# Kernel tuning notes

Hardware: AMD Instinct MI355X
Metric: run time of the kernel (lower is better)

The kernel has to match this reference:

```python
import jax, jax.numpy as jnp
import numpy as np

B, N, D = 2, 2048, 1024
H, HD = 16, 64
SCALE = HD ** (-0.5)


def setup_inputs() -> dict:
    key = jax.random.key(0)
    k1, k2, k3, k4 = jax.random.split(key, 4)
    x = jax.random.normal(k1, (B, N, D), dtype=jnp.float32)
    mask = jax.random.randint(k2, (B, 1, N, N), 0, 2) == 1  # bool, True = masked out
    W_qkv = jax.random.normal(k3, (D, 3 * H * HD), dtype=jnp.float32) * (D ** -0.5)
    W_out = jax.random.normal(k4, (H * HD, D), dtype=jnp.float32) * ((H * HD) ** -0.5)
    b_out = jnp.zeros((D,), dtype=jnp.float32)
    return {"x": x, "mask": mask, "W_qkv": W_qkv, "W_out": W_out, "b_out": b_out}


def reference(x, mask, W_qkv, W_out, b_out):
    b, n, _ = x.shape
    qkv = x @ W_qkv                                  # [b, n, 3*h*hd]
    q, k, v = jnp.split(qkv, 3, axis=-1)
    split_heads = lambda t: t.reshape(b, n, H, HD).transpose(0, 2, 1, 3)  # b h n d
    q, k, v = split_heads(q), split_heads(k), split_heads(v)
    scores = jnp.einsum('bhid,bhjd->bhij', q, k) * SCALE
    scores = jnp.where(mask, jnp.finfo(scores.dtype).min, scores)
    attn = jax.nn.softmax(scores, axis=-1)           # dropout p=0 -> identity
    out = jnp.einsum('bhij,bhjd->bhid', attn, v)     # [b, h, n, hd]
    out = out.transpose(0, 2, 1, 3).reshape(b, n, H * HD)
    return out @ W_out + b_out
```

## Files before the change

kernel.cpp:

```cpp
#include <hip/hip_runtime.h>
#include <stdint.h>

typedef unsigned short u16;
typedef short short8 __attribute__((ext_vector_type(8)));
typedef float f32x4 __attribute__((ext_vector_type(4)));
typedef float f32x16 __attribute__((ext_vector_type(16)));
typedef unsigned int uint2v __attribute__((ext_vector_type(2)));

#define K2E 0.18033688011112042f

__device__ __forceinline__ u16 f2bf(float f) {
  union { float f; uint32_t u; } v;
  v.f = f;
  uint32_t u = v.u;
  u += 0x7FFFu + ((u >> 16) & 1u);
  return (u16)(u >> 16);
}

__device__ __forceinline__ uint32_t cvtpk(float lo, float hi) {
  uint32_t r;
  asm("v_cvt_pk_bf16_f32 %0, %1, %2" : "=v"(r) : "v"(lo), "v"(hi));
  return r;
}

__device__ __forceinline__ float exp2a(float x) {
  float r;
  asm("v_exp_f32 %0, %1" : "=v"(r) : "v"(x));
  return r;
}

__device__ __forceinline__ float mask_keep(float p, uint32_t zm, int oc) {
  int m = (int)(zm << (31 - oc)) >> 31;
  return __uint_as_float(__float_as_uint(p) & (uint32_t)m);
}

__device__ __forceinline__ float row_add2(float x) {
  uint2v r = __builtin_amdgcn_permlane32_swap(__float_as_uint(x), __float_as_uint(x), false, false);
  return __uint_as_float(r.x) + __uint_as_float(r.y);
}

__device__ __forceinline__ void gld_lds16(const u16* src, char* dst) {
  __builtin_amdgcn_global_load_lds((const __attribute__((address_space(1))) void*)src,
                                   (__attribute__((address_space(3))) void*)dst, 16, 0, 0);
}

__device__ __forceinline__ void pack_frags(const f32x16& v, short8& fa, short8& fb) {
  union U { uint32_t w[4]; short8 v8; };
  uint32_t X0 = cvtpk(v[0], v[1]),   X1 = cvtpk(v[2], v[3]);
  uint32_t Y0 = cvtpk(v[4], v[5]),   Y1 = cvtpk(v[6], v[7]);
  uint32_t X2 = cvtpk(v[8], v[9]),   X3 = cvtpk(v[10], v[11]);
  uint32_t Y2 = cvtpk(v[12], v[13]), Y3 = cvtpk(v[14], v[15]);
  uint2v r0 = __builtin_amdgcn_permlane32_swap(X0, Y0, false, false);
  uint2v r1 = __builtin_amdgcn_permlane32_swap(X1, Y1, false, false);
  uint2v r2 = __builtin_amdgcn_permlane32_swap(X2, Y2, false, false);
  uint2v r3 = __builtin_amdgcn_permlane32_swap(X3, Y3, false, false);
  U ua; ua.w[0] = r0.x; ua.w[1] = r1.x; ua.w[2] = r0.y; ua.w[3] = r1.y; fa = ua.v8;
  U ub; ub.w[0] = r2.x; ub.w[1] = r3.x; ub.w[2] = r2.y; ub.w[3] = r3.y; fb = ub.v8;
}


__global__ __launch_bounds__(256) void k_cvt_x(const float* __restrict__ x,
                                               u16* __restrict__ xb, int n4) {
  int g = blockIdx.x * 256 + threadIdx.x;
  if (g >= n4) return;
  float4 v = ((const float4*)x)[g];
  ushort4 o;
  o.x = f2bf(v.x); o.y = f2bf(v.y); o.z = f2bf(v.z); o.w = f2bf(v.w);
  ((ushort4*)xb)[g] = o;
}

__global__ __launch_bounds__(256) void k_transpose_bf(const float* __restrict__ src,
                                                      u16* __restrict__ dst, int R, int C) {
  __shared__ float t[32][33];
  int c0 = blockIdx.x * 32, r0 = blockIdx.y * 32;
  int tx = threadIdx.x, ty = threadIdx.y;
#pragma unroll
  for (int i = 0; i < 4; ++i)
    t[ty + 8 * i][tx] = src[(size_t)(r0 + ty + 8 * i) * C + c0 + tx];
  __syncthreads();
#pragma unroll
  for (int i = 0; i < 4; ++i)
    dst[(size_t)(c0 + ty + 8 * i) * R + r0 + tx] = f2bf(t[tx][ty + 8 * i]);
}

__global__ __launch_bounds__(256) void k_mask_pack(const int* __restrict__ m,
                                                   uint32_t* __restrict__ w, int n) {
  int g = blockIdx.x * 256 + threadIdx.x;
  if (g >= n) return;
  unsigned long long bal = __ballot(m[g] != 0);
  int lane = threadIdx.x & 63;
  if (lane == 0) w[g >> 5] = (uint32_t)bal;
  else if (lane == 32) w[g >> 5] = (uint32_t)(bal >> 32);
}


#define GSTAGE(BUF, H, KT2)                                              \
  {                                                                      \
    char* dA_ = lds + (BUF) * 32768 + (H) * 16384 + (w << 11);           \
    const u16* a_ = As + (((KT2) << 6) + ((H) << 5));                    \
    const u16* b_ = Bs + (((KT2) << 6) + ((H) << 5));                    \
    gld_lds16(a_, dA_);                                                  \
    gld_lds16(a_ + (K << 4), dA_ + 1024);                                \
    gld_lds16(b_, dA_ + 8192);                                           \
    gld_lds16(b_ + (K << 4), dA_ + 9216);                                \
  }

#define PHASE(KT, H, VMS, DOSTAGE)                                                        \
  {                                                                                       \
    asm volatile("s_waitcnt vmcnt(" VMS ")" ::: "memory");                                \
    __builtin_amdgcn_sched_barrier(0);                                                    \
    __builtin_amdgcn_s_barrier();                                                         \
    __builtin_amdgcn_sched_barrier(0);                                                    \
    const char* rb_ = lds + ((KT) & 1) * 32768 + (H) * 16384;                             \
    short8 af[4], bfr[4];                                                                 \
    _Pragma("unroll")                                                                     \
    for (int mi = 0; mi < 4; ++mi) {                                                      \
      int row = wm * 64 + mi * 16 + lr;                                                   \
      af[mi] = *(const short8*)(rb_ + row * 64 + ((lg ^ ((row >> 1) & 3)) << 4));         \
    }                                                                                     \
    _Pragma("unroll")                                                                     \
    for (int ni = 0; ni < 4; ++ni) {                                                      \
      int row = wn * 64 + ni * 16 + lr;                                                   \
      bfr[ni] = *(const short8*)(rb_ + 8192 + row * 64 + ((lg ^ ((row >> 1) & 3)) << 4)); \
    }                                                                                     \
    asm volatile("s_waitcnt lgkmcnt(0)" ::: "memory");                                    \
    __builtin_amdgcn_sched_barrier(0);                                                    \
    __builtin_amdgcn_s_barrier();                                                         \
    __builtin_amdgcn_sched_barrier(0);                                                    \
    if (DOSTAGE) GSTAGE((KT) & 1, H, (KT) + 2);                                           \
    __builtin_amdgcn_s_setprio(1);                                                        \
    _Pragma("unroll")                                                                     \
    for (int mi = 0; mi < 4; ++mi)                                                        \
      _Pragma("unroll")                                                                   \
      for (int ni = 0; ni < 4; ++ni)                                                      \
        acc[mi][ni] =                                                                     \
            __builtin_amdgcn_mfma_f32_16x16x32_bf16(af[mi], bfr[ni], acc[mi][ni], 0, 0, 0); \
    __builtin_amdgcn_s_setprio(0);                                                        \
  }

__device__ __forceinline__ void gemm_core(const u16* __restrict__ A,
                                          const u16* __restrict__ Bt,
                                          int K, int m0, int n0,
                                          f32x4 (&acc)[4][4], char* lds) {
  const int t = threadIdx.x;
  const int l = t & 63;
  const int w = t >> 6;
  const int wm = w >> 1, wn = w & 1;
  const int lr = l & 15, lg = l >> 4;
  const int r0 = (w << 5) + (l >> 2);
  const int c = (l & 3) ^ ((r0 >> 1) & 3);
  const u16* As = A + (size_t)(m0 + r0) * K + c * 8;
  const u16* Bs = Bt + (size_t)(n0 + r0) * K + c * 8;
  const int nkt = K >> 6;

  GSTAGE(0, 0, 0);
  GSTAGE(0, 1, 0);
  GSTAGE(1, 0, 1);
  GSTAGE(1, 1, 1);

#pragma unroll 1
  for (int kt = 0; kt < nkt - 2; ++kt) {
    PHASE(kt, 0, "12", true);
    PHASE(kt, 1, "12", true);
  }
  PHASE(nkt - 2, 0, "12", false);
  PHASE(nkt - 2, 1, "8", false);
  PHASE(nkt - 1, 0, "4", false);
  PHASE(nkt - 1, 1, "0", false);
}

__global__ __launch_bounds__(256, 2) void k_gemm_qkv(const u16* __restrict__ xb,
                                                     const u16* __restrict__ wqT,
                                                     u16* __restrict__ Qb,
                                                     u16* __restrict__ Kb,
                                                     u16* __restrict__ VT) {
  __shared__ char lds[65536] __attribute__((aligned(128)));
  int n0 = blockIdx.x * 128, m0 = blockIdx.y * 128;
  f32x4 acc[4][4] = {};
  gemm_core(xb, wqT, 1024, m0, n0, acc, lds);
  const int l = threadIdx.x & 63, w = threadIdx.x >> 6;
  const int wm = w >> 1, wn = w & 1;
  const int lr = l & 15, lg = l >> 4;
#pragma unroll
  for (int mi = 0; mi < 4; ++mi)
#pragma unroll
    for (int ni = 0; ni < 4; ++ni)
#pragma unroll
      for (int r = 0; r < 4; ++r) {
        int m = m0 + wm * 64 + mi * 16 + lg * 4 + r;
        int n = n0 + wn * 64 + ni * 16 + lr;
        int b = m >> 11, seq = m & 2047;
        u16 v = f2bf(acc[mi][ni][r]);
        if (n < 1024) {
          Qb[((size_t)((b << 4) + (n >> 6)) * 2048 + seq) * 64 + (n & 63)] = v;
        } else if (n < 2048) {
          int nn = n - 1024;
          Kb[((size_t)((b << 4) + (nn >> 6)) * 2048 + seq) * 64 + (nn & 63)] = v;
        } else {
          int nn = n - 2048;
          VT[((size_t)((b << 4) + (nn >> 6)) * 64 + (nn & 63)) * 2048 + seq] = v;
        }
      }
}

__global__ __launch_bounds__(256, 2) void k_gemm_out(const u16* __restrict__ ao,
                                                     const u16* __restrict__ woT,
                                                     const float* __restrict__ bias,
                                                     float* __restrict__ out) {
  __shared__ char lds[65536] __attribute__((aligned(128)));
  int n0 = blockIdx.x * 128, m0 = blockIdx.y * 128;
  f32x4 acc[4][4] = {};
  gemm_core(ao, woT, 1024, m0, n0, acc, lds);
  const int l = threadIdx.x & 63, w = threadIdx.x >> 6;
  const int wm = w >> 1, wn = w & 1;
  const int lr = l & 15, lg = l >> 4;
#pragma unroll
  for (int mi = 0; mi < 4; ++mi)
#pragma unroll
    for (int ni = 0; ni < 4; ++ni)
#pragma unroll
      for (int r = 0; r < 4; ++r) {
        int m = m0 + wm * 64 + mi * 16 + lg * 4 + r;
        int n = n0 + wn * 64 + ni * 16 + lr;
        out[(size_t)m * 1024 + n] = acc[mi][ni][r] + bias[n];
      }
}

__global__ __launch_bounds__(512, 4) void k_attn(const u16* __restrict__ Qg,
                                                 const u16* __restrict__ Kg,
                                                 const u16* __restrict__ Vg,
                                                 const uint32_t* __restrict__ maskw,
                                                 u16* __restrict__ AO) {
  __shared__ char lds[65536] __attribute__((aligned(128)));
  const int bid = blockIdx.x;
  const int qt = bid & 15;
  const int hd = (bid >> 4) & 15;
  const int b = bid >> 8;
  const int bh = (b << 4) + hd;
  const int tx = threadIdx.x, l = tx & 63, w = tx >> 6;
  const int wq = w & 3, kvh = w >> 2;
  const int l31 = l & 31, h = l >> 5;
  const int hx4 = (h ^ (l & 7)) << 4;
  const int sc8 = ((l & 7) ^ (l >> 3)) << 3;
  const int lr8 = l >> 3;

  const u16* Qp = Qg + (size_t)bh * 131072;
  const int q = qt * 128 + wq * 32 + l31;
  const int kv0 = kvh << 10;

  const u16* kg = Kg + (size_t)bh * 131072 + (size_t)(kv0 + 16 * wq + lr8) * 64 + sc8;
  const u16* vg = Vg + (size_t)bh * 131072 + (size_t)(16 * wq + lr8) * 2048 + kv0 + sc8;
  const uint2v* mp = (const uint2v*)(maskw + ((size_t)(b << 11) + q) * 64) + (kvh << 4);

  short8 qf[4];
#pragma unroll
  for (int s = 0; s < 4; ++s)
    qf[s] = *(const short8*)(Qp + (size_t)q * 64 + s * 16 + h * 8);

  f32x16 Oa[2] = {};
  float l_run = 0.f;
  char* ldsH = lds + (kvh << 15);

#define STAGE(BSEL, TT)                                       \
  {                                                           \
    char* base_ = ldsH + (BSEL) * 16384 + (wq << 11);         \
    const u16* k_ = kg + ((size_t)(TT) << 12);                \
    const u16* v_ = vg + ((size_t)(TT) << 6);                 \
    gld_lds16(k_, base_);                                     \
    gld_lds16(k_ + 512, base_ + 1024);                        \
    gld_lds16(v_, base_ + 8192);                              \
    gld_lds16(v_ + 16384, base_ + 9216);                      \
  }

  STAGE(0, 0);

#pragma unroll 1
  for (int tt = 0; tt < 16; ++tt) {
    __syncthreads();
    if (tt + 1 < 16) STAGE((tt + 1) & 1, tt + 1);
    const uint2v mm = mp[tt];
    const char* kbase = ldsH + (tt & 1) * 16384 + l31 * 128;
    const char* vbase = kbase + 8192;

    f32x16 sa = {}, sb = {};
    __builtin_amdgcn_s_setprio(1);
#pragma unroll
    for (int s = 0; s < 4; ++s) {
      short8 k0 = *(const short8*)(kbase + ((s << 5) ^ hx4));
      short8 k1 = *(const short8*)(kbase + 4096 + ((s << 5) ^ hx4));
      sa = __builtin_amdgcn_mfma_f32_32x32x16_bf16(k0, qf[s], sa, 0, 0, 0);
      sb = __builtin_amdgcn_mfma_f32_32x32x16_bf16(k1, qf[s], sb, 0, 0, 0);
    }
    __builtin_amdgcn_s_setprio(0);

    const uint32_t zm0 = ~(mm.x >> (4 * h));
    const uint32_t zm1 = ~(mm.y >> (4 * h));
    float s0 = 0.f, s1 = 0.f, s2 = 0.f, s3 = 0.f;
#pragma unroll
    for (int r = 0; r < 16; r += 2) {
      const int oc = (r & 3) + 8 * (r >> 2);
      float e0 = mask_keep(exp2a(sa[r] * K2E), zm0, oc);
      float e1 = mask_keep(exp2a(sb[r] * K2E), zm1, oc);
      float e2 = mask_keep(exp2a(sa[r + 1] * K2E), zm0, oc + 1);
      float e3 = mask_keep(exp2a(sb[r + 1] * K2E), zm1, oc + 1);
      sa[r] = e0; sb[r] = e1; sa[r + 1] = e2; sb[r + 1] = e3;
      s0 += e0; s1 += e1; s2 += e2; s3 += e3;
    }
    l_run += row_add2((s0 + s2) + (s1 + s3));

    short8 pf[4];
    pack_frags(sa, pf[0], pf[1]);
    pack_frags(sb, pf[2], pf[3]);

    __builtin_amdgcn_s_setprio(1);
#pragma unroll
    for (int cc = 0; cc < 4; ++cc) {
      short8 v0 = *(const short8*)(vbase + ((cc << 5) ^ hx4));
      short8 v1 = *(const short8*)(vbase + 4096 + ((cc << 5) ^ hx4));
      Oa[0] = __builtin_amdgcn_mfma_f32_32x32x16_bf16(v0, pf[cc], Oa[0], 0, 0, 0);
      Oa[1] = __builtin_amdgcn_mfma_f32_32x32x16_bf16(v1, pf[cc], Oa[1], 0, 0, 0);
    }
    __builtin_amdgcn_s_setprio(0);
  }
#undef STAGE

  __syncthreads();
  float* cb = (float*)lds;
  if (kvh) {
#pragma unroll
    for (int r = 0; r < 32; ++r)
      cb[((wq << 5) + r) * 64 + l] = Oa[r >> 4][r & 15];
    cb[8192 + (wq << 6) + l] = l_run;
  }
  __syncthreads();
  if (!kvh) {
#pragma unroll
    for (int r = 0; r < 32; ++r)
      Oa[r >> 4][r & 15] += cb[((wq << 5) + r) * 64 + l];
    float lt = l_run + cb[8192 + (wq << 6) + l];
    float inv = 1.0f / fmaxf(lt, 1e-30f);
    u16* orow = AO + ((size_t)(b << 11) + q) * 1024 + hd * 64 + h * 4;
#pragma unroll
    for (int dt = 0; dt < 2; ++dt)
#pragma unroll
      for (int rq = 0; rq < 4; ++rq) {
        uint32_t w0 = cvtpk(Oa[dt][4 * rq + 0] * inv, Oa[dt][4 * rq + 1] * inv);
        uint32_t w1 = cvtpk(Oa[dt][4 * rq + 2] * inv, Oa[dt][4 * rq + 3] * inv);
        *(uint32_t*)(orow + dt * 32 + rq * 8) = w0;
        *(uint32_t*)(orow + dt * 32 + rq * 8 + 2) = w1;
      }
  }
}


extern "C" void kernel_launch(void* const* d_in, const int* in_sizes, int n_in,
                              void* d_out, int out_size, void* d_ws, size_t ws_size,
                              hipStream_t stream) {
  const float* x = (const float*)d_in[0];
  const int* mask = (const int*)d_in[1];
  const float* Wqkv = (const float*)d_in[2];
  const float* Wout = (const float*)d_in[3];
  const float* bout = (const float*)d_in[4];
  float* out = (float*)d_out;
  char* ws = (char*)d_ws;
  const size_t MB = 1u << 20;
  if (ws_size < 49 * MB) return;

  u16* xb = (u16*)(ws);
  u16* wqT = (u16*)(ws + 8 * MB);
  u16* woT = (u16*)(ws + 14 * MB);
  uint32_t* mw = (uint32_t*)(ws + 16 * MB);
  u16* Qb = (u16*)(ws + 17 * MB);
  u16* Kb = (u16*)(ws + 25 * MB);
  u16* VT = (u16*)(ws + 33 * MB);
  u16* AO = (u16*)(ws + 41 * MB);

  k_cvt_x<<<4096, 256, 0, stream>>>(x, xb, 1048576);
  k_transpose_bf<<<dim3(96, 32), dim3(32, 8), 0, stream>>>(Wqkv, wqT, 1024, 3072);
  k_transpose_bf<<<dim3(32, 32), dim3(32, 8), 0, stream>>>(Wout, woT, 1024, 1024);
  k_mask_pack<<<32768, 256, 0, stream>>>(mask, mw, 8388608);
  k_gemm_qkv<<<dim3(24, 32), 256, 0, stream>>>(xb, wqT, Qb, Kb, VT);
  k_attn<<<512, 512, 0, stream>>>(Qb, Kb, VT, mw, AO);
  k_gemm_out<<<dim3(8, 32), 256, 0, stream>>>(AO, woT, bout, out);
}
```

Measured before the change: 150.6 us.

## Triple-buffer GEMM pipeline, fold softmax scale into Q, compute row sums via MFMA

The GEMM core switches from a 2x2 half-tile double buffer to a three-stage ring of 16KB stages (48KB LDS) with occupancy raised to 3 blocks per CU. In attention, the exp2 scale factor is folded into Q at the QKV epilogue, masking uses a bfe+bfi pair, and softmax row sums are accumulated with an extra MFMA against a ones vector instead of VALU adds and a permlane swap. Together these target LDS-limited occupancy and VALU work in the softmax. In exchange the attention loop issues more MFMA work, Q rounding now includes the scale, and the GEMM loop hard-codes K=1024.

```diff
diff --git a/kernel.cpp b/kernel.cpp
--- a/kernel.cpp
+++ b/kernel.cpp
@@ -29,14 +29,11 @@
   return r;
 }
 
-__device__ __forceinline__ float mask_keep(float p, uint32_t zm, int oc) {
-  int m = (int)(zm << (31 - oc)) >> 31;
-  return __uint_as_float(__float_as_uint(p) & (uint32_t)m);
-}
-
-__device__ __forceinline__ float row_add2(float x) {
-  uint2v r = __builtin_amdgcn_permlane32_swap(__float_as_uint(x), __float_as_uint(x), false, false);
-  return __uint_as_float(r.x) + __uint_as_float(r.y);
+__device__ __forceinline__ float mask_zero(float p, uint32_t zm, int oc) {
+  int mext = __builtin_amdgcn_sbfe((int)zm, oc, 1);
+  float r;
+  asm("v_bfi_b32 %0, %1, 0, %2" : "=v"(r) : "v"(mext), "v"(p));
+  return r;
 }
 
 __device__ __forceinline__ void gld_lds16(const u16* src, char* dst) {
@@ -94,24 +91,24 @@
 }
 
 
-#define GSTAGE(BUF, H, KT2)                                              \
-  {                                                                      \
-    char* dA_ = lds + (BUF) * 32768 + (H) * 16384 + (w << 11);           \
-    const u16* a_ = As + (((KT2) << 6) + ((H) << 5));                    \
-    const u16* b_ = Bs + (((KT2) << 6) + ((H) << 5));                    \
-    gld_lds16(a_, dA_);                                                  \
-    gld_lds16(a_ + (K << 4), dA_ + 1024);                                \
-    gld_lds16(b_, dA_ + 8192);                                           \
-    gld_lds16(b_ + (K << 4), dA_ + 9216);                                \
-  }
-
-#define PHASE(KT, H, VMS, DOSTAGE)                                                        \
+#define GS(U, BUF)                                                   \
+  {                                                                  \
+    char* dA_ = lds + (BUF) * 16384 + (w << 11);                     \
+    const u16* a_ = As + ((U) << 5);                                 \
+    const u16* b_ = Bs + ((U) << 5);                                 \
+    gld_lds16(a_, dA_);                                              \
+    gld_lds16(a_ + (K << 4), dA_ + 1024);                            \
+    gld_lds16(b_, dA_ + 8192);                                       \
+    gld_lds16(b_ + (K << 4), dA_ + 9216);                            \
+  }
+
+#define PH(U, BUF, DOSTAGE, VMS)                                                          \
   {                                                                                       \
     asm volatile("s_waitcnt vmcnt(" VMS ")" ::: "memory");                                \
     __builtin_amdgcn_sched_barrier(0);                                                    \
     __builtin_amdgcn_s_barrier();                                                         \
     __builtin_amdgcn_sched_barrier(0);                                                    \
-    const char* rb_ = lds + ((KT) & 1) * 32768 + (H) * 16384;                             \
+    const char* rb_ = lds + (BUF) * 16384;                                                \
     short8 af[4], bfr[4];                                                                 \
     _Pragma("unroll")                                                                     \
     for (int mi = 0; mi < 4; ++mi) {                                                      \
@@ -127,7 +124,7 @@
     __builtin_amdgcn_sched_barrier(0);                                                    \
     __builtin_amdgcn_s_barrier();                                                         \
     __builtin_amdgcn_sched_barrier(0);                                                    \
-    if (DOSTAGE) GSTAGE((KT) & 1, H, (KT) + 2);                                           \
+    if (DOSTAGE) GS((U) + 3, BUF);                                                        \
     __builtin_amdgcn_s_setprio(1);                                                        \
     _Pragma("unroll")                                                                     \
     for (int mi = 0; mi < 4; ++mi)                                                        \
@@ -151,30 +148,31 @@
   const int c = (l & 3) ^ ((r0 >> 1) & 3);
   const u16* As = A + (size_t)(m0 + r0) * K + c * 8;
   const u16* Bs = Bt + (size_t)(n0 + r0) * K + c * 8;
-  const int nkt = K >> 6;
-
-  GSTAGE(0, 0, 0);
-  GSTAGE(0, 1, 0);
-  GSTAGE(1, 0, 1);
-  GSTAGE(1, 1, 1);
+
+  GS(0, 0);
+  GS(1, 1);
+  GS(2, 2);
 
 #pragma unroll 1
-  for (int kt = 0; kt < nkt - 2; ++kt) {
-    PHASE(kt, 0, "12", true);
-    PHASE(kt, 1, "12", true);
-  }
-  PHASE(nkt - 2, 0, "12", false);
-  PHASE(nkt - 2, 1, "8", false);
-  PHASE(nkt - 1, 0, "4", false);
-  PHASE(nkt - 1, 1, "0", false);
-}
-
-__global__ __launch_bounds__(256, 2) void k_gemm_qkv(const u16* __restrict__ xb,
+  for (int i = 0; i < 9; ++i) {
+    const int u = 3 * i;
+    PH(u + 0, 0, true, "8");
+    PH(u + 1, 1, true, "8");
+    PH(u + 2, 2, true, "8");
+  }
+  PH(27, 0, true, "8");
+  PH(28, 1, true, "8");
+  PH(29, 2, false, "8");
+  PH(30, 0, false, "4");
+  PH(31, 1, false, "0");
+}
+
+__global__ __launch_bounds__(256, 3) void k_gemm_qkv(const u16* __restrict__ xb,
                                                      const u16* __restrict__ wqT,
                                                      u16* __restrict__ Qb,
                                                      u16* __restrict__ Kb,
                                                      u16* __restrict__ VT) {
-  __shared__ char lds[65536] __attribute__((aligned(128)));
+  __shared__ char lds[49152] __attribute__((aligned(128)));
   int n0 = blockIdx.x * 128, m0 = blockIdx.y * 128;
   f32x4 acc[4][4] = {};
   gemm_core(xb, wqT, 1024, m0, n0, acc, lds);
@@ -190,24 +188,24 @@
         int m = m0 + wm * 64 + mi * 16 + lg * 4 + r;
         int n = n0 + wn * 64 + ni * 16 + lr;
         int b = m >> 11, seq = m & 2047;
-        u16 v = f2bf(acc[mi][ni][r]);
+        float av = acc[mi][ni][r];
         if (n < 1024) {
-          Qb[((size_t)((b << 4) + (n >> 6)) * 2048 + seq) * 64 + (n & 63)] = v;
+          Qb[((size_t)((b << 4) + (n >> 6)) * 2048 + seq) * 64 + (n & 63)] = f2bf(av * K2E);
         } else if (n < 2048) {
           int nn = n - 1024;
-          Kb[((size_t)((b << 4) + (nn >> 6)) * 2048 + seq) * 64 + (nn & 63)] = v;
+          Kb[((size_t)((b << 4) + (nn >> 6)) * 2048 + seq) * 64 + (nn & 63)] = f2bf(av);
         } else {
           int nn = n - 2048;
-          VT[((size_t)((b << 4) + (nn >> 6)) * 64 + (nn & 63)) * 2048 + seq] = v;
+          VT[((size_t)((b << 4) + (nn >> 6)) * 64 + (nn & 63)) * 2048 + seq] = f2bf(av);
         }
       }
 }
 
-__global__ __launch_bounds__(256, 2) void k_gemm_out(const u16* __restrict__ ao,
+__global__ __launch_bounds__(256, 3) void k_gemm_out(const u16* __restrict__ ao,
                                                      const u16* __restrict__ woT,
                                                      const float* __restrict__ bias,
                                                      float* __restrict__ out) {
-  __shared__ char lds[65536] __attribute__((aligned(128)));
+  __shared__ char lds[49152] __attribute__((aligned(128)));
   int n0 = blockIdx.x * 128, m0 = blockIdx.y * 128;
   f32x4 acc[4][4] = {};
   gemm_core(ao, woT, 1024, m0, n0, acc, lds);
@@ -257,8 +255,9 @@
   for (int s = 0; s < 4; ++s)
     qf[s] = *(const short8*)(Qp + (size_t)q * 64 + s * 16 + h * 8);
 
+  const short8 ones8 = {0x3F80, 0x3F80, 0x3F80, 0x3F80, 0x3F80, 0x3F80, 0x3F80, 0x3F80};
   f32x16 Oa[2] = {};
-  float l_run = 0.f;
+  f32x16 acc_l = {};
   char* ldsH = lds + (kvh << 15);
 
 #define STAGE(BSEL, TT)                                       \
@@ -293,20 +292,14 @@
     }
     __builtin_amdgcn_s_setprio(0);
 
-    const uint32_t zm0 = ~(mm.x >> (4 * h));
-    const uint32_t zm1 = ~(mm.y >> (4 * h));
-    float s0 = 0.f, s1 = 0.f, s2 = 0.f, s3 = 0.f;
-#pragma unroll
-    for (int r = 0; r < 16; r += 2) {
+    const uint32_t zm0 = mm.x >> (4 * h);
+    const uint32_t zm1 = mm.y >> (4 * h);
+#pragma unroll
+    for (int r = 0; r < 16; ++r) {
       const int oc = (r & 3) + 8 * (r >> 2);
-      float e0 = mask_keep(exp2a(sa[r] * K2E), zm0, oc);
-      float e1 = mask_keep(exp2a(sb[r] * K2E), zm1, oc);
-      float e2 = mask_keep(exp2a(sa[r + 1] * K2E), zm0, oc + 1);
-      float e3 = mask_keep(exp2a(sb[r + 1] * K2E), zm1, oc + 1);
-      sa[r] = e0; sb[r] = e1; sa[r + 1] = e2; sb[r + 1] = e3;
-      s0 += e0; s1 += e1; s2 += e2; s3 += e3;
+      sa[r] = mask_zero(exp2a(sa[r]), zm0, oc);
+      sb[r] = mask_zero(exp2a(sb[r]), zm1, oc);
     }
-    l_run += row_add2((s0 + s2) + (s1 + s3));
 
     short8 pf[4];
     pack_frags(sa, pf[0], pf[1]);
@@ -319,6 +312,7 @@
       short8 v1 = *(const short8*)(vbase + 4096 + ((cc << 5) ^ hx4));
       Oa[0] = __builtin_amdgcn_mfma_f32_32x32x16_bf16(v0, pf[cc], Oa[0], 0, 0, 0);
       Oa[1] = __builtin_amdgcn_mfma_f32_32x32x16_bf16(v1, pf[cc], Oa[1], 0, 0, 0);
+      acc_l = __builtin_amdgcn_mfma_f32_32x32x16_bf16(ones8, pf[cc], acc_l, 0, 0, 0);
     }
     __builtin_amdgcn_s_setprio(0);
   }
@@ -330,14 +324,14 @@
 #pragma unroll
     for (int r = 0; r < 32; ++r)
       cb[((wq << 5) + r) * 64 + l] = Oa[r >> 4][r & 15];
-    cb[8192 + (wq << 6) + l] = l_run;
+    cb[8192 + (wq << 6) + l] = acc_l[0];
   }
   __syncthreads();
   if (!kvh) {
 #pragma unroll
     for (int r = 0; r < 32; ++r)
       Oa[r >> 4][r & 15] += cb[((wq << 5) + r) * 64 + l];
-    float lt = l_run + cb[8192 + (wq << 6) + l];
+    float lt = acc_l[0] + cb[8192 + (wq << 6) + l];
     float inv = 1.0f / fmaxf(lt, 1e-30f);
     u16* orow = AO + ((size_t)(b << 11) + q) * 1024 + hd * 64 + h * 4;
 #pragma unroll
```

After: 136.5 us. 1.1x faster.
